# Performance work log

Measured on AMD Instinct MI355X. Metric: run time of the kernel, lower is better.

## Reference

```python
import jax, jax.numpy as jnp
import numpy as np
from jax import lax

B, N, C = 2, 4096, 128
HEADS = 4
HD = C // HEADS
EXP = 2  # FFN_expand
EPS = 1e-5


def layernorm(x, w, b):
    mu = jnp.mean(x, axis=-1, keepdims=True)
    var = jnp.mean(jnp.square(x - mu), axis=-1, keepdims=True)
    return (x - mu) * lax.rsqrt(var + EPS) * w + b


def conv2d(x, w, b, pad, groups=1):
    # x: [B, Cin, H, W], w: [Cout, Cin//groups, kh, kw]
    y = lax.conv_general_dilated(
        x, w, window_strides=(1, 1), padding=[(pad, pad), (pad, pad)],
        dimension_numbers=('NCHW', 'OIHW', 'NCHW'), feature_group_count=groups)
    return y + b[None, :, None, None]


def setup_inputs() -> dict:
    key = jax.random.key(0)
    ks = jax.random.split(key, 16)
    C2 = C * EXP
    inp = {
        'x': jax.random.normal(ks[0], (B, N, C), jnp.float32),
        'H': 64,
        'W': 64,
        'ln1_w': jnp.ones((C,), jnp.float32),
        'ln1_b': jnp.zeros((C,), jnp.float32),
        'q_w': jax.random.normal(ks[1], (C, C), jnp.float32) * 0.02,
        'kv_w': jax.random.normal(ks[2], (2 * C, C), jnp.float32) * 0.02,
        'proj_w': jax.random.normal(ks[3], (C, C), jnp.float32) * 0.02,
        'proj_b': jnp.zeros((C,), jnp.float32),
        'ln2_w': jnp.ones((C,), jnp.float32),
        'ln2_b': jnp.zeros((C,), jnp.float32),
        'conv1_w': jax.random.normal(ks[4], (C2, C, 1, 1), jnp.float32) * np.sqrt(2.0 / C2),
        'conv1_b': jnp.zeros((C2,), jnp.float32),
        'conv33_w': jax.random.normal(ks[5], (C2, 1, 3, 3), jnp.float32) * np.sqrt(2.0 / 9),
        'conv33_b': jnp.zeros((C2,), jnp.float32),
        'conv55_w': jax.random.normal(ks[6], (C2, 1, 5, 5), jnp.float32) * np.sqrt(2.0 / 25),
        'conv55_b': jnp.zeros((C2,), jnp.float32),
        'conv4_w': jax.random.normal(ks[7], (C, C, 1, 1), jnp.float32) * np.sqrt(2.0 / C),
        'conv4_b': jnp.zeros((C,), jnp.float32),
    }
    return inp


def reference(x, H, W, ln1_w, ln1_b, q_w, kv_w, proj_w, proj_b,
              ln2_w, ln2_b, conv1_w, conv1_b, conv33_w, conv33_b,
              conv55_w, conv55_b, conv4_w, conv4_b):
    b, n, c = x.shape
    scale = HD ** -0.5

    # ---- Multi-head self-attention (sr_ratio=1) ----
    h = layernorm(x, ln1_w, ln1_b)
    q = jnp.einsum('bnc,oc->bno', h, q_w).reshape(b, n, HEADS, HD).transpose(0, 2, 1, 3)
    kv = jnp.einsum('bnc,oc->bno', h, kv_w).reshape(b, n, 2, HEADS, HD).transpose(2, 0, 3, 1, 4)
    k, v = kv[0], kv[1]
    attn = jnp.einsum('bhqd,bhkd->bhqk', q, k) * scale  # [B, heads, N, N]
    attn = jax.nn.softmax(attn, axis=-1)
    out = jnp.einsum('bhqk,bhkd->bhqd', attn, v).transpose(0, 2, 1, 3).reshape(b, n, c)
    out = jnp.einsum('bnc,oc->bno', out, proj_w) + proj_b
    x = x + out

    # ---- MFFN: conv1 + (dw3x3 + dw5x5) branches, SimpleGate, conv4 ----
    h = layernorm(x, ln2_w, ln2_b)
    hc = h.reshape(b, H, W, c).transpose(0, 3, 1, 2)  # NCHW
    x1 = conv2d(hc, conv1_w, conv1_b, pad=0)
    x33 = conv2d(x1, conv33_w, conv33_b, pad=1, groups=c * EXP)
    x55 = conv2d(x1, conv55_w, conv55_b, pad=2, groups=c * EXP)
    s = x1 + x33 + x55
    a, g = jnp.split(s, 2, axis=1)  # SimpleGate
    gated = a * g
    y = conv2d(gated, conv4_w, conv4_b, pad=0)
    y = y.transpose(0, 2, 3, 1).reshape(b, H * W, c)
    return x + y
```

## Files before the change

### kernel.cpp

```cpp
#include <hip/hip_runtime.h>
#include <hip/hip_bf16.h>
#include <math.h>

#define NB 2
#define NN 4096
#define NC 128
#define NH 4
#define HD 32
#define C2 256
#define HW 64
#define EPS 1e-5f

typedef unsigned short u16;
typedef short bf16x8 __attribute__((ext_vector_type(8)));
typedef unsigned short u16x8 __attribute__((ext_vector_type(8)));
typedef float f32x16 __attribute__((ext_vector_type(16)));

__device__ __forceinline__ u16 f2b(float x) {
    return __bfloat16_as_ushort(__float2bfloat16(x));
}
__device__ __forceinline__ float b2f(u16 v) {
    return __uint_as_float((unsigned)v << 16);
}
__device__ __forceinline__ unsigned pack_bf16(float a, float b) {
    return (unsigned)f2b(a) | ((unsigned)f2b(b) << 16);
}
__device__ __forceinline__ f32x16 fzero16() {
    f32x16 z;
    #pragma unroll
    for (int i = 0; i < 16; ++i) z[i] = 0.f;
    return z;
}
union U32x4 { unsigned u[4]; bf16x8 v; };

__device__ __forceinline__ void plswap(unsigned& a, unsigned& b) {
    asm("v_permlane32_swap_b32 %0, %1" : "+v"(a), "+v"(b));
}

__global__ void k_prep(const float* __restrict__ q_w, const float* __restrict__ kv_w,
                       const float* __restrict__ proj_w, const float* __restrict__ c1_w,
                       const float* __restrict__ c4_w, const float* __restrict__ c33_w,
                       const float* __restrict__ c55_w, const float* __restrict__ c33_b,
                       const float* __restrict__ c55_b,
                       u16* wqkv, u16* wproj, u16* wc1, u16* wc4,
                       u16* weff, float* beff) {
    const int tid = blockIdx.x * blockDim.x + threadIdx.x;
    const int nth = gridDim.x * blockDim.x;
    const float s = 0.17677669529663687f * 1.4426950408889634f;
    for (int i = tid; i < 128 * 128; i += nth) wqkv[i] = f2b(q_w[i] * s);
    for (int i = tid; i < 256 * 128; i += nth) wqkv[128 * 128 + i] = f2b(kv_w[i]);
    for (int i = tid; i < 128 * 128; i += nth) wproj[i] = f2b(proj_w[i]);
    for (int i = tid; i < 256 * 128; i += nth) wc1[i] = f2b(c1_w[i]);
    for (int i = tid; i < 128 * 128; i += nth) wc4[i] = f2b(c4_w[i]);
    for (int i = tid; i < 25 * 256; i += nth) {
        const int k = i / 256, c = i % 256;
        const int dy = k / 5 - 2, dx = k % 5 - 2;
        float w = c55_w[c * 25 + k];
        if (dy >= -1 && dy <= 1 && dx >= -1 && dx <= 1)
            w += c33_w[c * 9 + (dy + 1) * 3 + (dx + 1)];
        if (k == 12) w += 1.0f;
        weff[k * 256 + c] = f2b(w);
    }
    for (int i = tid; i < 256; i += nth) beff[i] = c33_b[i] + c55_b[i];
}

__global__ __launch_bounds__(256) void k_ln(
    const float* __restrict__ x, const float* __restrict__ w, const float* __restrict__ b,
    u16* __restrict__ h) {
    const int l = threadIdx.x & 63, wid = threadIdx.x >> 6;
    const int row = blockIdx.x * 4 + wid;
    const float2 xv = *(const float2*)(x + (size_t)row * NC + l * 2);
    float sum = xv.x + xv.y, ss = xv.x * xv.x + xv.y * xv.y;
    #pragma unroll
    for (int off = 1; off < 64; off <<= 1) {
        sum += __shfl_xor(sum, off);
        ss  += __shfl_xor(ss, off);
    }
    const float mean = sum * (1.0f / NC);
    const float var  = ss * (1.0f / NC) - mean * mean;
    const float rstd = rsqrtf(var + EPS);
    const float2 wv = *(const float2*)(w + l * 2);
    const float2 bv = *(const float2*)(b + l * 2);
    const float h0 = (xv.x - mean) * rstd * wv.x + bv.x;
    const float h1 = (xv.y - mean) * rstd * wv.y + bv.y;
    *(unsigned*)(h + (size_t)row * NC + l * 2) = pack_bf16(h0, h1);
}

__device__ __forceinline__ f32x16 gemm_tile_32x32(
    const u16* __restrict__ A, const u16* __restrict__ W, int m0, int n0, int q, int h5) {
    const u16* ap = A + (size_t)(m0 + q) * 128 + h5 * 8;
    const u16* wp = W + (size_t)(n0 + q) * 128 + h5 * 8;
    f32x16 acc = fzero16();
    #pragma unroll
    for (int kk = 0; kk < 8; ++kk) {
        bf16x8 af = *(const bf16x8*)(ap + kk * 16);
        bf16x8 wf = *(const bf16x8*)(wp + kk * 16);
        acc = __builtin_amdgcn_mfma_f32_32x32x16_bf16(af, wf, acc, 0, 0, 0);
    }
    return acc;
}
#define GEMM_PROLOG(NCOLS)                                    \
    const int l = threadIdx.x & 63, wid = threadIdx.x >> 6;   \
    const int q = l & 31, h5 = l >> 5;                        \
    const int m0 = blockIdx.x * 64 + (wid >> 1) * 32;         \
    const int n0 = blockIdx.y * 64 + (wid & 1) * 32;          \
    const int o = n0 + q;                                     \
    (void)o;

__global__ __launch_bounds__(256) void k_gemm_qkv(
    const u16* __restrict__ h1, const u16* __restrict__ wqkv,
    u16* __restrict__ qb, u16* __restrict__ kbuf, u16* __restrict__ vtb) {
    GEMM_PROLOG(384)
    f32x16 acc = gemm_tile_32x32(h1, wqkv, m0, n0, q, h5);
    if (o < 256) {
        #pragma unroll
        for (int r = 0; r < 16; ++r) {
            const int mr = m0 + (r & 3) + 8 * (r >> 2) + 4 * h5;
            const int b_ = mr >> 12, n = mr & 4095;
            const u16 val = f2b(acc[r]);
            if (o < 128) {
                qb[((size_t)(b_ * 4 + (o >> 5)) * NN + n) * HD + (o & 31)] = val;
            } else {
                const int o2 = o - 128;
                kbuf[((size_t)(b_ * 4 + (o2 >> 5)) * NN + n) * HD + (o2 & 31)] = val;
            }
        }
    } else {
        const int vo = o - 256;
        const int hh = vo >> 5, d = vo & 31;
        u16* vrow = vtb + ((size_t)((m0 >> 12) * 4 + hh) * 32 + d) * NN;
        const int nb = (m0 & 4095) + 4 * h5;
        #pragma unroll
        for (int g = 0; g < 4; ++g) {
            ushort4 pv;
            pv.x = f2b(acc[4 * g + 0]); pv.y = f2b(acc[4 * g + 1]);
            pv.z = f2b(acc[4 * g + 2]); pv.w = f2b(acc[4 * g + 3]);
            *(ushort4*)(vrow + nb + 8 * g) = pv;
        }
    }
}

__global__ __launch_bounds__(256, 4) void k_attn(
    const u16* __restrict__ qb, const u16* __restrict__ kbuf, const u16* __restrict__ vtb,
    u16* __restrict__ ctxb) {
    __shared__ float sl[4][32];
    __shared__ float so[4][64][17];

    const int l = threadIdx.x & 63, w = threadIdx.x >> 6;
    const int q = l & 31, h5 = l >> 5;
    const int bh = blockIdx.x;
    const int qbase = blockIdx.y * 32;

    const u16* qp = qb + ((size_t)bh * NN + qbase + q) * HD + h5 * 8;
    const bf16x8 qf0 = *(const bf16x8*)qp;
    const bf16x8 qf1 = *(const bf16x8*)(qp + 16);

    bf16x8 ones;
    #pragma unroll
    for (int i = 0; i < 8; ++i) ones[i] = (short)0x3F80;

    const int kb0 = w * 1024;
    const u16* kp = kbuf + ((size_t)bh * NN + kb0 + q) * HD + h5 * 8;
    const u16* vp = vtb + ((size_t)bh * 32 + q) * NN + kb0 + h5 * 8;

    f32x16 O = fzero16();
    f32x16 L = fzero16();

    for (int t = 0; t < 32; ++t) {
        const bf16x8 kf0 = *(const bf16x8*)kp;
        const bf16x8 kf1 = *(const bf16x8*)(kp + 16);
        const bf16x8 vf0 = *(const bf16x8*)vp;
        const bf16x8 vf1 = *(const bf16x8*)(vp + 16);
        kp += 32 * HD;
        vp += 32;

        f32x16 s = fzero16();
        s = __builtin_amdgcn_mfma_f32_32x32x16_bf16(kf0, qf0, s, 0, 0, 0);
        s = __builtin_amdgcn_mfma_f32_32x32x16_bf16(kf1, qf1, s, 0, 0, 0);

        float p[16];
        #pragma unroll
        for (int r = 0; r < 16; ++r) p[r] = __builtin_amdgcn_exp2f(s[r]);

        unsigned pk[8];
        #pragma unroll
        for (int i = 0; i < 8; ++i) pk[i] = pack_bf16(p[2 * i], p[2 * i + 1]);
        U32x4 a0, a1;
        {
            unsigned x0 = pk[0], x2 = pk[2]; plswap(x0, x2);
            unsigned x1 = pk[1], x3 = pk[3]; plswap(x1, x3);
            a0.u[0] = x0; a0.u[1] = x1; a0.u[2] = x2; a0.u[3] = x3;
            unsigned y0 = pk[4], y2 = pk[6]; plswap(y0, y2);
            unsigned y1 = pk[5], y3 = pk[7]; plswap(y1, y3);
            a1.u[0] = y0; a1.u[1] = y1; a1.u[2] = y2; a1.u[3] = y3;
        }
        O = __builtin_amdgcn_mfma_f32_32x32x16_bf16(a0.v, vf0, O, 0, 0, 0);
        O = __builtin_amdgcn_mfma_f32_32x32x16_bf16(a1.v, vf1, O, 0, 0, 0);
        L = __builtin_amdgcn_mfma_f32_32x32x16_bf16(a0.v, ones, L, 0, 0, 0);
        L = __builtin_amdgcn_mfma_f32_32x32x16_bf16(a1.v, ones, L, 0, 0, 0);
    }

    if (q == 0) {
        #pragma unroll
        for (int r = 0; r < 16; ++r) sl[w][(r & 3) + 8 * (r >> 2) + 4 * h5] = L[r];
    }
    #pragma unroll
    for (int r = 0; r < 16; ++r) so[w][l][r] = O[r];
    __syncthreads();

    const int b_ = bh >> 2, h_ = bh & 3;
    #pragma unroll
    for (int i = 0; i < 4; ++i) {
        const int r = 4 * w + i;
        const int qr = (r & 3) + 8 * (r >> 2) + 4 * h5;
        const float os = so[0][l][r] + so[1][l][r] + so[2][l][r] + so[3][l][r];
        const float Lq = sl[0][qr] + sl[1][qr] + sl[2][qr] + sl[3][qr];
        ctxb[((size_t)(b_ * NN + qbase + qr)) * NC + h_ * 32 + q] = f2b(os / Lq);
    }
}

__global__ __launch_bounds__(256) void k_proj_ln(
    const u16* __restrict__ ctxb, const u16* __restrict__ wproj,
    const float* __restrict__ pbias, const float* __restrict__ x,
    const float* __restrict__ lnw, const float* __restrict__ lnb,
    float* __restrict__ x2, u16* __restrict__ h2) {
    __shared__ float sx[32][129];
    const int l = threadIdx.x & 63, wid = threadIdx.x >> 6;
    const int q = l & 31, h5 = l >> 5;
    const int m0 = blockIdx.x * 32;
    const int n0 = wid * 32;
    const int o = n0 + q;

    f32x16 acc = gemm_tile_32x32(ctxb, wproj, m0, n0, q, h5);
    const float bo = pbias[o];
    #pragma unroll
    for (int r = 0; r < 16; ++r) {
        const int rr = (r & 3) + 8 * (r >> 2) + 4 * h5;
        const int mr = m0 + rr;
        const float xv = acc[r] + bo + x[(size_t)mr * NC + o];
        x2[(size_t)mr * NC + o] = xv;
        sx[rr][o] = xv;
    }
    __syncthreads();

    const int t = threadIdx.x;
    const int row = t >> 3, cs = (t & 7) * 16;
    float vals[16];
    float sum = 0.f, ss = 0.f;
    #pragma unroll
    for (int i = 0; i < 16; ++i) {
        const float v = sx[row][cs + i];
        vals[i] = v; sum += v; ss += v * v;
    }
    #pragma unroll
    for (int off = 1; off < 8; off <<= 1) {
        sum += __shfl_xor(sum, off);
        ss  += __shfl_xor(ss, off);
    }
    const float mean = sum * (1.0f / NC);
    const float var  = ss * (1.0f / NC) - mean * mean;
    const float rstd = rsqrtf(var + EPS);
    const size_t base = (size_t)(m0 + row) * NC + cs;
    #pragma unroll
    for (int i = 0; i < 16; i += 2) {
        const float h0 = (vals[i]     - mean) * rstd * lnw[cs + i]     + lnb[cs + i];
        const float h1 = (vals[i + 1] - mean) * rstd * lnw[cs + i + 1] + lnb[cs + i + 1];
        *(unsigned*)(h2 + base + i) = pack_bf16(h0, h1);
    }
}

__global__ __launch_bounds__(256) void k_gemm_c1(
    const u16* __restrict__ h2, const u16* __restrict__ wc1,
    const float* __restrict__ bias, u16* __restrict__ x1) {
    GEMM_PROLOG(256)
    f32x16 acc = gemm_tile_32x32(h2, wc1, m0, n0, q, h5);
    const float bo = bias[o];
    #pragma unroll
    for (int r = 0; r < 16; ++r) {
        const int mr = m0 + (r & 3) + 8 * (r >> 2) + 4 * h5;
        x1[(size_t)mr * 256 + o] = f2b(acc[r] + bo);
    }
}

__global__ __launch_bounds__(256) void k_dwgate(
    const u16* __restrict__ x1, const u16* __restrict__ weff, const float* __restrict__ beff,
    u16* __restrict__ gatedb) {
    const int t = threadIdx.x;
    const int cg = (t & 31) * 4;
    const int pb = blockIdx.x * 8 + (t >> 5);
    const int b_ = pb >> 12, p = pb & 4095;
    const int py = p >> 6, px = p & 63;
    const u16* base = x1 + ((size_t)b_ * 4096 + p) * C2;

    float a0 = 0.f, a1 = 0.f, a2 = 0.f, a3 = 0.f;
    float g0 = 0.f, g1 = 0.f, g2 = 0.f, g3 = 0.f;
    #pragma unroll
    for (int dy = -2; dy <= 2; ++dy) {
        const int yy = py + dy;
        const bool yin = (yy >= 0) && (yy < HW);
        #pragma unroll
        for (int dx = -2; dx <= 2; ++dx) {
            const int xx = px + dx;
            const bool in = yin && (xx >= 0) && (xx < HW);
            const int k5 = (dy + 2) * 5 + (dx + 2);
            const u16* xp = base + (dy * HW + dx) * C2;
            ushort4 xa = in ? *(const ushort4*)(xp + cg) : ushort4{0, 0, 0, 0};
            ushort4 xg = in ? *(const ushort4*)(xp + 128 + cg) : ushort4{0, 0, 0, 0};
            const ushort4 wa = *(const ushort4*)(weff + k5 * 256 + cg);
            const ushort4 wg = *(const ushort4*)(weff + k5 * 256 + 128 + cg);
            a0 += b2f(xa.x) * b2f(wa.x); a1 += b2f(xa.y) * b2f(wa.y);
            a2 += b2f(xa.z) * b2f(wa.z); a3 += b2f(xa.w) * b2f(wa.w);
            g0 += b2f(xg.x) * b2f(wg.x); g1 += b2f(xg.y) * b2f(wg.y);
            g2 += b2f(xg.z) * b2f(wg.z); g3 += b2f(xg.w) * b2f(wg.w);
        }
    }
    const float4 ba = *(const float4*)(beff + cg);
    const float4 bg = *(const float4*)(beff + 128 + cg);
    ushort4 o4;
    o4.x = f2b((a0 + ba.x) * (g0 + bg.x));
    o4.y = f2b((a1 + ba.y) * (g1 + bg.y));
    o4.z = f2b((a2 + ba.z) * (g2 + bg.z));
    o4.w = f2b((a3 + ba.w) * (g3 + bg.w));
    *(ushort4*)(gatedb + (size_t)pb * 128 + cg) = o4;
}

__global__ __launch_bounds__(256) void k_gemm_c4(
    const u16* __restrict__ gatedb, const u16* __restrict__ wc4,
    const float* __restrict__ bias, const float* __restrict__ x2, float* __restrict__ out) {
    GEMM_PROLOG(128)
    f32x16 acc = gemm_tile_32x32(gatedb, wc4, m0, n0, q, h5);
    const float bo = bias[o];
    #pragma unroll
    for (int r = 0; r < 16; ++r) {
        const int mr = m0 + (r & 3) + 8 * (r >> 2) + 4 * h5;
        out[(size_t)mr * 128 + o] = acc[r] + bo + x2[(size_t)mr * 128 + o];
    }
}

extern "C" void kernel_launch(void* const* d_in, const int* in_sizes, int n_in,
                              void* d_out, int out_size, void* d_ws, size_t ws_size,
                              hipStream_t stream) {
    const float* x      = (const float*)d_in[0];
    const float* ln1_w  = (const float*)d_in[3];
    const float* ln1_b  = (const float*)d_in[4];
    const float* q_w    = (const float*)d_in[5];
    const float* kv_w   = (const float*)d_in[6];
    const float* proj_w = (const float*)d_in[7];
    const float* proj_b = (const float*)d_in[8];
    const float* ln2_w  = (const float*)d_in[9];
    const float* ln2_b  = (const float*)d_in[10];
    const float* c1_w   = (const float*)d_in[11];
    const float* c1_b   = (const float*)d_in[12];
    const float* c33_w  = (const float*)d_in[13];
    const float* c33_b  = (const float*)d_in[14];
    const float* c55_w  = (const float*)d_in[15];
    const float* c55_b  = (const float*)d_in[16];
    const float* c4_w   = (const float*)d_in[17];
    const float* c4_b   = (const float*)d_in[18];

    char* p = (char*)d_ws;
    u16*   wqkv  = (u16*)p;   p += 384 * 128 * 2;
    u16*   wproj = (u16*)p;   p += 128 * 128 * 2;
    u16*   wc1   = (u16*)p;   p += 256 * 128 * 2;
    u16*   wc4   = (u16*)p;   p += 128 * 128 * 2;
    u16*   weff  = (u16*)p;   p += 25 * 256 * 2;
    float* beff  = (float*)p; p += 256 * 4;
    p = (char*)(((size_t)p + 255) & ~(size_t)255);
    u16*   h1    = (u16*)p;   p += (size_t)8192 * 128 * 2;
    u16*   qb    = (u16*)p;   p += (size_t)8 * 4096 * 32 * 2;
    u16*   kb    = (u16*)p;   p += (size_t)8 * 4096 * 32 * 2;
    u16*   vtb   = (u16*)p;   p += (size_t)8 * 32 * 4096 * 2;
    u16*   ctxb  = (u16*)p;   p += (size_t)8192 * 128 * 2;
    float* x2    = (float*)p; p += (size_t)8192 * 128 * 4;
    u16*   h2    = (u16*)p;   p += (size_t)8192 * 128 * 2;
    u16*   x1    = (u16*)p;   p += (size_t)8192 * 256 * 2;
    u16*   gatedb= (u16*)p;   p += (size_t)8192 * 128 * 2;
    float* out   = (float*)d_out;

    k_prep<<<64, 256, 0, stream>>>(q_w, kv_w, proj_w, c1_w, c4_w, c33_w, c55_w,
                                   c33_b, c55_b, wqkv, wproj, wc1, wc4, weff, beff);
    k_ln<<<2048, 256, 0, stream>>>(x, ln1_w, ln1_b, h1);
    k_gemm_qkv<<<dim3(128, 6), 256, 0, stream>>>(h1, wqkv, qb, kb, vtb);
    k_attn<<<dim3(NB * NH, NN / 32), 256, 0, stream>>>(qb, kb, vtb, ctxb);
    k_proj_ln<<<256, 256, 0, stream>>>(ctxb, wproj, proj_b, x, ln2_w, ln2_b, x2, h2);
    k_gemm_c1<<<dim3(128, 4), 256, 0, stream>>>(h2, wc1, c1_b, x1);
    k_dwgate<<<1024, 256, 0, stream>>>(x1, weff, beff, gatedb);
    k_gemm_c4<<<dim3(128, 2), 256, 0, stream>>>(gatedb, wc4, c4_b, x2, out);
}
```

Measured before the change: 221.8 us.

## Fuse prep+LN, VALU row-sum and K/V prefetch in attention, interior dwconv path

Merges the weight-prep and first layernorm kernels into a single launch. In attention, replaces the ones-matrix MFMAs used for the softmax denominator with VALU sums plus a cross-half lane swap, and prefetches the next K/V fragments one iteration ahead. The depthwise gate kernel gains a specialised interior path that skips the bounds checks. The trade-off is extra VALU work and register pressure in the attention loop and duplicated code in the depthwise kernel.

```diff
diff --git a/kernel.cpp b/kernel.cpp
--- a/kernel.cpp
+++ b/kernel.cpp
@@ -36,16 +36,44 @@
 __device__ __forceinline__ void plswap(unsigned& a, unsigned& b) {
     asm("v_permlane32_swap_b32 %0, %1" : "+v"(a), "+v"(b));
 }
-
-__global__ void k_prep(const float* __restrict__ q_w, const float* __restrict__ kv_w,
-                       const float* __restrict__ proj_w, const float* __restrict__ c1_w,
-                       const float* __restrict__ c4_w, const float* __restrict__ c33_w,
-                       const float* __restrict__ c55_w, const float* __restrict__ c33_b,
-                       const float* __restrict__ c55_b,
-                       u16* wqkv, u16* wproj, u16* wc1, u16* wc4,
-                       u16* weff, float* beff) {
-    const int tid = blockIdx.x * blockDim.x + threadIdx.x;
-    const int nth = gridDim.x * blockDim.x;
+__device__ __forceinline__ float xswap(float v, int h5) {
+    float a = v, b = v;
+    asm("v_permlane32_swap_b32 %0, %1" : "+v"(a), "+v"(b));
+    return h5 ? a : b;
+}
+
+__global__ __launch_bounds__(256) void k_prep_ln(
+    const float* __restrict__ q_w, const float* __restrict__ kv_w,
+    const float* __restrict__ proj_w, const float* __restrict__ c1_w,
+    const float* __restrict__ c4_w, const float* __restrict__ c33_w,
+    const float* __restrict__ c55_w, const float* __restrict__ c33_b,
+    const float* __restrict__ c55_b,
+    u16* wqkv, u16* wproj, u16* wc1, u16* wc4,
+    u16* weff, float* beff,
+    const float* __restrict__ x, const float* __restrict__ ln1w,
+    const float* __restrict__ ln1b, u16* __restrict__ h1) {
+    if (blockIdx.x < 2048) {
+        const int l = threadIdx.x & 63, wid = threadIdx.x >> 6;
+        const int row = blockIdx.x * 4 + wid;
+        const float2 xv = *(const float2*)(x + (size_t)row * NC + l * 2);
+        float sum = xv.x + xv.y, ss = xv.x * xv.x + xv.y * xv.y;
+        #pragma unroll
+        for (int off = 1; off < 64; off <<= 1) {
+            sum += __shfl_xor(sum, off);
+            ss  += __shfl_xor(ss, off);
+        }
+        const float mean = sum * (1.0f / NC);
+        const float var  = ss * (1.0f / NC) - mean * mean;
+        const float rstd = rsqrtf(var + EPS);
+        const float2 wv = *(const float2*)(ln1w + l * 2);
+        const float2 bv = *(const float2*)(ln1b + l * 2);
+        const float h0 = (xv.x - mean) * rstd * wv.x + bv.x;
+        const float h1v = (xv.y - mean) * rstd * wv.y + bv.y;
+        *(unsigned*)(h1 + (size_t)row * NC + l * 2) = pack_bf16(h0, h1v);
+        return;
+    }
+    const int tid = (blockIdx.x - 2048) * 256 + threadIdx.x;
+    const int nth = 64 * 256;
     const float s = 0.17677669529663687f * 1.4426950408889634f;
     for (int i = tid; i < 128 * 128; i += nth) wqkv[i] = f2b(q_w[i] * s);
     for (int i = tid; i < 256 * 128; i += nth) wqkv[128 * 128 + i] = f2b(kv_w[i]);
@@ -64,28 +92,6 @@
     for (int i = tid; i < 256; i += nth) beff[i] = c33_b[i] + c55_b[i];
 }
 
-__global__ __launch_bounds__(256) void k_ln(
-    const float* __restrict__ x, const float* __restrict__ w, const float* __restrict__ b,
-    u16* __restrict__ h) {
-    const int l = threadIdx.x & 63, wid = threadIdx.x >> 6;
-    const int row = blockIdx.x * 4 + wid;
-    const float2 xv = *(const float2*)(x + (size_t)row * NC + l * 2);
-    float sum = xv.x + xv.y, ss = xv.x * xv.x + xv.y * xv.y;
-    #pragma unroll
-    for (int off = 1; off < 64; off <<= 1) {
-        sum += __shfl_xor(sum, off);
-        ss  += __shfl_xor(ss, off);
-    }
-    const float mean = sum * (1.0f / NC);
-    const float var  = ss * (1.0f / NC) - mean * mean;
-    const float rstd = rsqrtf(var + EPS);
-    const float2 wv = *(const float2*)(w + l * 2);
-    const float2 bv = *(const float2*)(b + l * 2);
-    const float h0 = (xv.x - mean) * rstd * wv.x + bv.x;
-    const float h1 = (xv.y - mean) * rstd * wv.y + bv.y;
-    *(unsigned*)(h + (size_t)row * NC + l * 2) = pack_bf16(h0, h1);
-}
-
 __device__ __forceinline__ f32x16 gemm_tile_32x32(
     const u16* __restrict__ A, const u16* __restrict__ W, int m0, int n0, int q, int h5) {
     const u16* ap = A + (size_t)(m0 + q) * 128 + h5 * 8;
@@ -155,24 +161,25 @@
     const bf16x8 qf0 = *(const bf16x8*)qp;
     const bf16x8 qf1 = *(const bf16x8*)(qp + 16);
 
-    bf16x8 ones;
-    #pragma unroll
-    for (int i = 0; i < 8; ++i) ones[i] = (short)0x3F80;
-
     const int kb0 = w * 1024;
     const u16* kp = kbuf + ((size_t)bh * NN + kb0 + q) * HD + h5 * 8;
     const u16* vp = vtb + ((size_t)bh * 32 + q) * NN + kb0 + h5 * 8;
 
     f32x16 O = fzero16();
-    f32x16 L = fzero16();
+    float lacc = 0.f;
+
+    bf16x8 kf0 = *(const bf16x8*)kp;
+    bf16x8 kf1 = *(const bf16x8*)(kp + 16);
+    bf16x8 vf0 = *(const bf16x8*)vp;
+    bf16x8 vf1 = *(const bf16x8*)(vp + 16);
 
     for (int t = 0; t < 32; ++t) {
-        const bf16x8 kf0 = *(const bf16x8*)kp;
-        const bf16x8 kf1 = *(const bf16x8*)(kp + 16);
-        const bf16x8 vf0 = *(const bf16x8*)vp;
-        const bf16x8 vf1 = *(const bf16x8*)(vp + 16);
-        kp += 32 * HD;
-        vp += 32;
+        const u16* kpn = kp + ((t < 31) ? 32 * HD : 0);
+        const u16* vpn = vp + ((t < 31) ? 32 : 0);
+        const bf16x8 nk0 = *(const bf16x8*)kpn;
+        const bf16x8 nk1 = *(const bf16x8*)(kpn + 16);
+        const bf16x8 nv0 = *(const bf16x8*)vpn;
+        const bf16x8 nv1 = *(const bf16x8*)(vpn + 16);
 
         f32x16 s = fzero16();
         s = __builtin_amdgcn_mfma_f32_32x32x16_bf16(kf0, qf0, s, 0, 0, 0);
@@ -181,6 +188,16 @@
         float p[16];
         #pragma unroll
         for (int r = 0; r < 16; ++r) p[r] = __builtin_amdgcn_exp2f(s[r]);
+
+        {
+            const float s0 = (p[0] + p[1]) + (p[2] + p[3]);
+            const float s1 = (p[4] + p[5]) + (p[6] + p[7]);
+            const float s2 = (p[8] + p[9]) + (p[10] + p[11]);
+            const float s3 = (p[12] + p[13]) + (p[14] + p[15]);
+            float ls = (s0 + s1) + (s2 + s3);
+            ls += xswap(ls, h5);
+            lacc += ls;
+        }
 
         unsigned pk[8];
         #pragma unroll
@@ -196,14 +213,12 @@
         }
         O = __builtin_amdgcn_mfma_f32_32x32x16_bf16(a0.v, vf0, O, 0, 0, 0);
         O = __builtin_amdgcn_mfma_f32_32x32x16_bf16(a1.v, vf1, O, 0, 0, 0);
-        L = __builtin_amdgcn_mfma_f32_32x32x16_bf16(a0.v, ones, L, 0, 0, 0);
-        L = __builtin_amdgcn_mfma_f32_32x32x16_bf16(a1.v, ones, L, 0, 0, 0);
-    }
-
-    if (q == 0) {
-        #pragma unroll
-        for (int r = 0; r < 16; ++r) sl[w][(r & 3) + 8 * (r >> 2) + 4 * h5] = L[r];
-    }
+
+        kf0 = nk0; kf1 = nk1; vf0 = nv0; vf1 = nv1;
+        kp = kpn; vp = vpn;
+    }
+
+    if (l < 32) sl[w][l] = lacc;
     #pragma unroll
     for (int r = 0; r < 16; ++r) so[w][l][r] = O[r];
     __syncthreads();
@@ -282,26 +297,20 @@
     }
 }
 
-__global__ __launch_bounds__(256) void k_dwgate(
-    const u16* __restrict__ x1, const u16* __restrict__ weff, const float* __restrict__ beff,
-    u16* __restrict__ gatedb) {
-    const int t = threadIdx.x;
-    const int cg = (t & 31) * 4;
-    const int pb = blockIdx.x * 8 + (t >> 5);
-    const int b_ = pb >> 12, p = pb & 4095;
-    const int py = p >> 6, px = p & 63;
-    const u16* base = x1 + ((size_t)b_ * 4096 + p) * C2;
-
-    float a0 = 0.f, a1 = 0.f, a2 = 0.f, a3 = 0.f;
-    float g0 = 0.f, g1 = 0.f, g2 = 0.f, g3 = 0.f;
+template<bool CHK>
+__device__ __forceinline__ void dw_accum(
+    const u16* __restrict__ base, const u16* __restrict__ weff,
+    int py, int px, int cg,
+    float& a0, float& a1, float& a2, float& a3,
+    float& g0, float& g1, float& g2, float& g3) {
     #pragma unroll
     for (int dy = -2; dy <= 2; ++dy) {
         const int yy = py + dy;
-        const bool yin = (yy >= 0) && (yy < HW);
+        const bool yin = !CHK || ((yy >= 0) && (yy < HW));
         #pragma unroll
         for (int dx = -2; dx <= 2; ++dx) {
             const int xx = px + dx;
-            const bool in = yin && (xx >= 0) && (xx < HW);
+            const bool in = !CHK || (yin && (xx >= 0) && (xx < HW));
             const int k5 = (dy + 2) * 5 + (dx + 2);
             const u16* xp = base + (dy * HW + dx) * C2;
             ushort4 xa = in ? *(const ushort4*)(xp + cg) : ushort4{0, 0, 0, 0};
@@ -313,6 +322,27 @@
             g0 += b2f(xg.x) * b2f(wg.x); g1 += b2f(xg.y) * b2f(wg.y);
             g2 += b2f(xg.z) * b2f(wg.z); g3 += b2f(xg.w) * b2f(wg.w);
         }
+    }
+}
+
+__global__ __launch_bounds__(256) void k_dwgate(
+    const u16* __restrict__ x1, const u16* __restrict__ weff, const float* __restrict__ beff,
+    u16* __restrict__ gatedb) {
+    const int t = threadIdx.x;
+    const int cg = (t & 31) * 4;
+    const int pb = blockIdx.x * 8 + (t >> 5);
+    const int b_ = pb >> 12, p = pb & 4095;
+    const int py = p >> 6, px = p & 63;
+    const int px0 = (blockIdx.x * 8) & 63;
+    const u16* base = x1 + ((size_t)b_ * 4096 + p) * C2;
+
+    float a0 = 0.f, a1 = 0.f, a2 = 0.f, a3 = 0.f;
+    float g0 = 0.f, g1 = 0.f, g2 = 0.f, g3 = 0.f;
+    const bool interior = (py >= 2) && (py < 62) && (px0 >= 8) && (px0 <= 48);
+    if (interior) {
+        dw_accum<false>(base, weff, py, px, cg, a0, a1, a2, a3, g0, g1, g2, g3);
+    } else {
+        dw_accum<true>(base, weff, py, px, cg, a0, a1, a2, a3, g0, g1, g2, g3);
     }
     const float4 ba = *(const float4*)(beff + cg);
     const float4 bg = *(const float4*)(beff + 128 + cg);
@@ -377,9 +407,9 @@
     u16*   gatedb= (u16*)p;   p += (size_t)8192 * 128 * 2;
     float* out   = (float*)d_out;
 
-    k_prep<<<64, 256, 0, stream>>>(q_w, kv_w, proj_w, c1_w, c4_w, c33_w, c55_w,
-                                   c33_b, c55_b, wqkv, wproj, wc1, wc4, weff, beff);
-    k_ln<<<2048, 256, 0, stream>>>(x, ln1_w, ln1_b, h1);
+    k_prep_ln<<<2112, 256, 0, stream>>>(q_w, kv_w, proj_w, c1_w, c4_w, c33_w, c55_w,
+                                        c33_b, c55_b, wqkv, wproj, wc1, wc4, weff, beff,
+                                        x, ln1_w, ln1_b, h1);
     k_gemm_qkv<<<dim3(128, 6), 256, 0, stream>>>(h1, wqkv, qb, kb, vtb);
     k_attn<<<dim3(NB * NH, NN / 32), 256, 0, stream>>>(qb, kb, vtb, ctxb);
     k_proj_ln<<<256, 256, 0, stream>>>(ctxb, wproj, proj_b, x, ln2_w, ln2_b, x2, h2);
```

New measurement: 220.1 us. No clear change (-0.8%).
